# Performance work log

Hardware: AMD Instinct MI355X
Metric: run time of the kernel (lower is better)

## Reference

```python
import jax, jax.numpy as jnp
import numpy as np

NEG_INF = -1e6

def setup_inputs() -> dict:
    key = jax.random.key(0)
    ks = jax.random.split(key, 7)
    B, Q, K, D, H = 16, 64, 1024, 256, 128
    return {
        "queries": jax.random.normal(ks[0], (B, Q, D), dtype=jnp.float32),
        "keys": jax.random.normal(ks[1], (B, K, D), dtype=jnp.float32),
        "values": jax.random.normal(ks[2], (B, K, D), dtype=jnp.float32),
        "valid_lens": jax.random.randint(ks[3], (B,), 1, K + 1, dtype=jnp.int32),
        "W_q": jax.random.normal(ks[4], (D, H), dtype=jnp.float32) * (1.0 / np.sqrt(D)),
        "W_k": jax.random.normal(ks[5], (D, H), dtype=jnp.float32) * (1.0 / np.sqrt(D)),
        "w_v": jax.random.normal(ks[6], (H,), dtype=jnp.float32) * (1.0 / np.sqrt(H)),
    }

def reference(queries, keys, values, valid_lens, W_q, W_k, w_v):
    # project: [B,Q,H], [B,K,H]
    q = jnp.einsum('bqd,dh->bqh', queries, W_q)
    k = jnp.einsum('bkd,dh->bkh', keys, W_k)
    # broadcast add -> tanh -> score: [B,Q,K]
    features = jnp.tanh(q[:, :, None, :] + k[:, None, :, :])  # [B,Q,K,H]
    scores = jnp.einsum('bqkh,h->bqk', features, w_v)
    # masked softmax over key axis (valid_lens per batch)
    K_len = keys.shape[1]
    mask = jnp.arange(K_len)[None, None, :] < valid_lens[:, None, None]  # [B,1,K]
    scores = jnp.where(mask, scores, NEG_INF)
    attn = jax.nn.softmax(scores, axis=-1)
    # weighted sum of values: [B,Q,Dv]  (dropout p=0 -> identity)
    return jnp.einsum('bqk,bkd->bqd', attn, values)
```

## Files before the change

### kernel.cpp

```cpp
#include <hip/hip_runtime.h>

#define DDIM 256
#define HDIM 128
#define KLEN 1024
#define SCL 2.8853900817779268f

__global__ __launch_bounds__(256) void proj_kernel(
    const float* __restrict__ queries, const float* __restrict__ keys,
    const float* __restrict__ W_q, const float* __restrict__ W_k,
    float* __restrict__ Eq, float* __restrict__ Ek)
{
    __shared__ union {
        float a[64 * 64];
        float t[32][68];
    } sm;

    const int tid  = threadIdx.x;
    const int lane = tid & 63;
    const int wav  = tid >> 6;

    int blk = blockIdx.x;
    bool iskey; int b = 0, kc0 = 0, hb, row0;
    const float* in; const float* W;
    if (blk < 1024) {
        iskey = true;
        int xcd = blk & 7, s = blk >> 3;
        b = ((s >> 6) << 3) | xcd;
        int r6 = s & 63;
        kc0 = (r6 >> 2) << 6;
        hb  = (r6 & 3) << 5;
        row0 = b * KLEN + kc0;
        in = keys; W = W_k;
    } else {
        iskey = false;
        int qrb = blk - 1024;
        row0 = (qrb >> 2) << 6;
        hb   = (qrb & 3) << 5;
        in = queries; W = W_q;
    }

    const int hg8 = __builtin_amdgcn_readfirstlane(wav << 3);
    const float* Wu = W + hb + hg8;

    const int srow = tid >> 4;
    const int sgd  = tid & 15;
    const float* gsrc = in + (size_t)(row0 + srow) * DDIM + (sgd << 2);

    float4 pf0 = *(const float4*)(gsrc);
    float4 pf1 = *(const float4*)(gsrc + 16 * DDIM);
    float4 pf2 = *(const float4*)(gsrc + 32 * DDIM);
    float4 pf3 = *(const float4*)(gsrc + 48 * DDIM);

    float acc[8];
    #pragma unroll
    for (int c = 0; c < 8; c++) acc[c] = 0.f;

    const int w0 = (srow)      * 64 + ((sgd ^ ((srow)      & 7)) << 2);
    const int w1 = (srow + 16) * 64 + ((sgd ^ ((srow + 16) & 7)) << 2);
    const int w2 = (srow + 32) * 64 + ((sgd ^ ((srow + 32) & 7)) << 2);
    const int w3 = (srow + 48) * 64 + ((sgd ^ ((srow + 48) & 7)) << 2);

    for (int dt0 = 0; dt0 < DDIM; dt0 += 64) {
        *(float4*)(sm.a + w0) = pf0;
        *(float4*)(sm.a + w1) = pf1;
        *(float4*)(sm.a + w2) = pf2;
        *(float4*)(sm.a + w3) = pf3;
        __syncthreads();
        if (dt0 < DDIM - 64) {
            const float* g2 = gsrc + dt0 + 64;
            pf0 = *(const float4*)(g2);
            pf1 = *(const float4*)(g2 + 16 * DDIM);
            pf2 = *(const float4*)(g2 + 32 * DDIM);
            pf3 = *(const float4*)(g2 + 48 * DDIM);
        }
        const float* arow = sm.a + lane * 64;
        const int lx = lane & 7;
        #pragma unroll
        for (int d4 = 0; d4 < 64; d4 += 4) {
            float4 a = *(const float4*)(arow + ((((d4 >> 2)) ^ lx) << 2));
            const float* wr = Wu + (size_t)(dt0 + d4) * HDIM;
            #pragma unroll
            for (int c = 0; c < 8; c++) acc[c] = fmaf(a.x, wr[c],            acc[c]);
            #pragma unroll
            for (int c = 0; c < 8; c++) acc[c] = fmaf(a.y, wr[HDIM + c],     acc[c]);
            #pragma unroll
            for (int c = 0; c < 8; c++) acc[c] = fmaf(a.z, wr[2 * HDIM + c], acc[c]);
            #pragma unroll
            for (int c = 0; c < 8; c++) acc[c] = fmaf(a.w, wr[3 * HDIM + c], acc[c]);
        }
        __syncthreads();
    }

    float e[8];
    #pragma unroll
    for (int c = 0; c < 8; c++) e[c] = __builtin_amdgcn_exp2f(SCL * acc[c]);

    if (!iskey) {
        float* dst = Eq + (size_t)(row0 + lane) * HDIM + hb + hg8;
        *(float4*)(dst)     = make_float4(e[0], e[1], e[2], e[3]);
        *(float4*)(dst + 4) = make_float4(e[4], e[5], e[6], e[7]);
    } else {
        #pragma unroll
        for (int c = 0; c < 8; c++) sm.t[(wav << 3) + c][lane] = e[c];
        __syncthreads();
        float* dstb = Ek + (size_t)b * HDIM * KLEN + (size_t)hb * KLEN + kc0;
        #pragma unroll
        for (int i = 0; i < 2; i++) {
            int g = tid + (i << 8);
            int h = g >> 4, k4 = (g & 15) << 2;
            float4 o = *(const float4*)(&sm.t[h][k4]);
            *(float4*)(dstb + (size_t)h * KLEN + k4) = o;
        }
    }
}

__global__ __launch_bounds__(256) void score_av_kernel(
    const float* __restrict__ Eq, const float* __restrict__ Ek,
    const float* __restrict__ w_v, const int* __restrict__ valid_lens,
    const float* __restrict__ values,
    float* __restrict__ part, float* __restrict__ Tp)
{
    __shared__ union {
        struct {
            float4 eqw[4][HDIM];
            float  el[128][8];
        } p;
        float4 slab[4][8][64];
    } sm;
    __shared__ float tslab[4][8];

    const int tid = threadIdx.x;
    const int lane = tid & 63, wav = tid >> 6;
    int blk = blockIdx.x;
    int xcd = blk & 7, s = blk >> 3;
    int b = ((s >> 6) << 3) | xcd;
    int r = s & 63;
    int qt = r >> 3, kq = r & 7;
    int bq0 = b * 64 + qt * 8;
    int k0g = kq << 7;
    int vlen = valid_lens[b];

    #pragma unroll
    for (int i = 0; i < 2; i++) {
        int slot = tid + (i << 8);
        int w = slot >> 7, h = slot & 127;
        sm.p.eqw[w][h] = make_float4(
            Eq[(size_t)(bq0 + 2 * w) * HDIM + h],
            Eq[(size_t)(bq0 + 2 * w + 1) * HDIM + h],
            -2.0f * w_v[h], 0.f);
    }
    __syncthreads();

    const int kl = lane << 1;
    const float* ekp = Ek + (size_t)b * HDIM * KLEN + k0g + kl;
    float2 buf[8];
    #pragma unroll
    for (int j = 0; j < 8; j++)
        buf[j] = *(const float2*)(ekp + (size_t)j * KLEN);

    float2 acc0 = make_float2(0.f, 0.f), acc1 = make_float2(0.f, 0.f);
    for (int h0 = 0; h0 < HDIM; h0 += 8) {
        float2 nxt[8];
        if (h0 < HDIM - 8) {
            #pragma unroll
            for (int j = 0; j < 8; j++)
                nxt[j] = *(const float2*)(ekp + (size_t)(h0 + 8 + j) * KLEN);
        }
        #pragma unroll
        for (int j = 0; j < 8; j++) {
            float4 e = sm.p.eqw[wav][h0 + j];
            float2 ek = buf[j];
            acc0.x = fmaf(e.z, __builtin_amdgcn_rcpf(fmaf(e.x, ek.x, 1.f)), acc0.x);
            acc0.y = fmaf(e.z, __builtin_amdgcn_rcpf(fmaf(e.x, ek.y, 1.f)), acc0.y);
            acc1.x = fmaf(e.z, __builtin_amdgcn_rcpf(fmaf(e.y, ek.x, 1.f)), acc1.x);
            acc1.y = fmaf(e.z, __builtin_amdgcn_rcpf(fmaf(e.y, ek.y, 1.f)), acc1.y);
        }
        #pragma unroll
        for (int j = 0; j < 8; j++) buf[j] = nxt[j];
    }

    {
        int kg = k0g + kl;
        float e00 = (kg     < vlen) ? __expf(acc0.x) : 0.f;
        float e01 = (kg + 1 < vlen) ? __expf(acc0.y) : 0.f;
        float e10 = (kg     < vlen) ? __expf(acc1.x) : 0.f;
        float e11 = (kg + 1 < vlen) ? __expf(acc1.y) : 0.f;
        *(float2*)(&sm.p.el[kl][2 * wav])     = make_float2(e00, e10);
        *(float2*)(&sm.p.el[kl + 1][2 * wav]) = make_float2(e01, e11);
    }
    __syncthreads();

    int kw = wav << 5;
    int kg0 = k0g + kw;
    int cnt = vlen - kg0; cnt = cnt < 0 ? 0 : (cnt > 32 ? 32 : cnt);
    int cnt4 = (cnt + 3) & ~3;
    const float* vb = values + ((size_t)b * KLEN + kg0) * DDIM + (lane << 2);

    float4 acc[8];
    float acct[8];
    #pragma unroll
    for (int q = 0; q < 8; q++) { acc[q] = make_float4(0.f, 0.f, 0.f, 0.f); acct[q] = 0.f; }

    for (int k = 0; k < cnt4; k += 4) {
        #pragma unroll
        for (int j = 0; j < 4; j++) {
            float4 v  = *(const float4*)(vb + (size_t)(k + j) * DDIM);
            float4 p0 = *(const float4*)(&sm.p.el[kw + k + j][0]);
            float4 p1 = *(const float4*)(&sm.p.el[kw + k + j][4]);
            float pq[8] = {p0.x, p0.y, p0.z, p0.w, p1.x, p1.y, p1.z, p1.w};
            #pragma unroll
            for (int q = 0; q < 8; q++) {
                acc[q].x = fmaf(pq[q], v.x, acc[q].x);
                acc[q].y = fmaf(pq[q], v.y, acc[q].y);
                acc[q].z = fmaf(pq[q], v.z, acc[q].z);
                acc[q].w = fmaf(pq[q], v.w, acc[q].w);
                acct[q] += pq[q];
            }
        }
    }

    __syncthreads();
    #pragma unroll
    for (int q = 0; q < 8; q++) sm.slab[wav][q][lane] = acc[q];
    if (lane == 0) {
        #pragma unroll
        for (int q = 0; q < 8; q++) tslab[wav][q] = acct[q];
    }
    __syncthreads();
    #pragma unroll
    for (int e = 0; e < 2; e++) {
        int slot = (tid << 1) | e;
        int q = slot >> 6, d4 = slot & 63;
        float4 a = sm.slab[0][q][d4];
        #pragma unroll
        for (int g = 1; g < 4; g++) {
            float4 t = sm.slab[g][q][d4];
            a.x += t.x; a.y += t.y; a.z += t.z; a.w += t.w;
        }
        *(float4*)(part + ((size_t)kq * 1024 + bq0 + q) * DDIM + (d4 << 2)) = a;
    }
    if (tid < 8) {
        float t = tslab[0][tid] + tslab[1][tid] + tslab[2][tid] + tslab[3][tid];
        Tp[(size_t)kq * 1024 + bq0 + tid] = t;
    }
}

__global__ __launch_bounds__(256) void combine_kernel(
    const float* __restrict__ part, const float* __restrict__ Tp,
    float* __restrict__ out)
{
    int i = blockIdx.x * 256 + threadIdx.x;
    int row = i >> 6;
    const float4* p4 = (const float4*)part;
    float t = 0.f;
    #pragma unroll
    for (int j = 0; j < 8; j++) t += Tp[(size_t)j * 1024 + row];
    float inv = 1.0f / t;
    float4 a = p4[i];
    #pragma unroll
    for (int j = 1; j < 8; j++) {
        float4 v = p4[(size_t)j * 65536 + i];
        a.x += v.x; a.y += v.y; a.z += v.z; a.w += v.w;
    }
    a.x *= inv; a.y *= inv; a.z *= inv; a.w *= inv;
    ((float4*)out)[i] = a;
}

extern "C" void kernel_launch(void* const* d_in, const int* in_sizes, int n_in,
                              void* d_out, int out_size, void* d_ws, size_t ws_size,
                              hipStream_t stream) {
    const float* queries    = (const float*)d_in[0];
    const float* keys       = (const float*)d_in[1];
    const float* values     = (const float*)d_in[2];
    const int*   valid_lens = (const int*)d_in[3];
    const float* W_q        = (const float*)d_in[4];
    const float* W_k        = (const float*)d_in[5];
    const float* w_v        = (const float*)d_in[6];

    float* Eq   = (float*)d_ws;
    float* Ek   = Eq + 131072;
    float* part = Ek + 2097152;
    float* Tp   = part + 2097152;

    proj_kernel<<<1088, 256, 0, stream>>>(queries, keys, W_q, W_k, Eq, Ek);
    score_av_kernel<<<1024, 256, 0, stream>>>(Eq, Ek, w_v, valid_lens, values, part, Tp);
    combine_kernel<<<256, 256, 0, stream>>>(part, Tp, (float*)d_out);
}
```

Before: 136.2 us.

## Halve queries per score block, double grid, skip fully masked key chunks

The score/AV kernel now handles 4 queries per block instead of 8 and launches twice as many blocks, with a launch-bounds occupancy hint of 8 blocks. Blocks whose key chunk lies entirely past valid_len write zeros and exit early, skipping the tanh-score and value work. The cross-wave reduction becomes a serialized accumulate into shared memory with extra barriers, and each block now reloads its Ek and values tiles for half as many queries, which doubles that global traffic.

```diff
diff --git a/kernel.cpp b/kernel.cpp
--- a/kernel.cpp
+++ b/kernel.cpp
@@ -114,40 +114,44 @@
     }
 }
 
-__global__ __launch_bounds__(256) void score_av_kernel(
+__global__ __launch_bounds__(256, 8) void score_av_kernel(
     const float* __restrict__ Eq, const float* __restrict__ Ek,
     const float* __restrict__ w_v, const int* __restrict__ valid_lens,
     const float* __restrict__ values,
     float* __restrict__ part, float* __restrict__ Tp)
 {
     __shared__ union {
-        struct {
-            float4 eqw[4][HDIM];
-            float  el[128][8];
-        } p;
-        float4 slab[4][8][64];
-    } sm;
-    __shared__ float tslab[4][8];
+        float2 eqw[4][HDIM];
+        float  accbuf[4][256];
+    } u;
+    __shared__ float el[128][8];
+    __shared__ float tacc[4];
 
     const int tid = threadIdx.x;
     const int lane = tid & 63, wav = tid >> 6;
     int blk = blockIdx.x;
     int xcd = blk & 7, s = blk >> 3;
-    int b = ((s >> 6) << 3) | xcd;
-    int r = s & 63;
+    int b = ((s >> 7) << 3) | xcd;
+    int r = s & 127;
     int qt = r >> 3, kq = r & 7;
-    int bq0 = b * 64 + qt * 8;
+    int bq0 = b * 64 + qt * 4;
     int k0g = kq << 7;
     int vlen = valid_lens[b];
+
+    if (k0g >= vlen) {
+        int q = tid >> 6, d4 = tid & 63;
+        *(float4*)(part + ((size_t)kq * 1024 + bq0 + q) * DDIM + (d4 << 2)) =
+            make_float4(0.f, 0.f, 0.f, 0.f);
+        if (tid < 4) Tp[(size_t)kq * 1024 + bq0 + tid] = 0.f;
+        return;
+    }
 
     #pragma unroll
     for (int i = 0; i < 2; i++) {
         int slot = tid + (i << 8);
         int w = slot >> 7, h = slot & 127;
-        sm.p.eqw[w][h] = make_float4(
-            Eq[(size_t)(bq0 + 2 * w) * HDIM + h],
-            Eq[(size_t)(bq0 + 2 * w + 1) * HDIM + h],
-            -2.0f * w_v[h], 0.f);
+        u.eqw[w][h] = make_float2(Eq[(size_t)(bq0 + w) * HDIM + h],
+                                  -2.0f * w_v[h]);
     }
     __syncthreads();
 
@@ -158,7 +162,7 @@
     for (int j = 0; j < 8; j++)
         buf[j] = *(const float2*)(ekp + (size_t)j * KLEN);
 
-    float2 acc0 = make_float2(0.f, 0.f), acc1 = make_float2(0.f, 0.f);
+    float accx = 0.f, accy = 0.f;
     for (int h0 = 0; h0 < HDIM; h0 += 8) {
         float2 nxt[8];
         if (h0 < HDIM - 8) {
@@ -168,12 +172,10 @@
         }
         #pragma unroll
         for (int j = 0; j < 8; j++) {
-            float4 e = sm.p.eqw[wav][h0 + j];
+            float2 e  = u.eqw[wav][h0 + j];
             float2 ek = buf[j];
-            acc0.x = fmaf(e.z, __builtin_amdgcn_rcpf(fmaf(e.x, ek.x, 1.f)), acc0.x);
-            acc0.y = fmaf(e.z, __builtin_amdgcn_rcpf(fmaf(e.x, ek.y, 1.f)), acc0.y);
-            acc1.x = fmaf(e.z, __builtin_amdgcn_rcpf(fmaf(e.y, ek.x, 1.f)), acc1.x);
-            acc1.y = fmaf(e.z, __builtin_amdgcn_rcpf(fmaf(e.y, ek.y, 1.f)), acc1.y);
+            accx = fmaf(e.y, __builtin_amdgcn_rcpf(fmaf(e.x, ek.x, 1.f)), accx);
+            accy = fmaf(e.y, __builtin_amdgcn_rcpf(fmaf(e.x, ek.y, 1.f)), accy);
         }
         #pragma unroll
         for (int j = 0; j < 8; j++) buf[j] = nxt[j];
@@ -181,35 +183,29 @@
 
     {
         int kg = k0g + kl;
-        float e00 = (kg     < vlen) ? __expf(acc0.x) : 0.f;
-        float e01 = (kg + 1 < vlen) ? __expf(acc0.y) : 0.f;
-        float e10 = (kg     < vlen) ? __expf(acc1.x) : 0.f;
-        float e11 = (kg + 1 < vlen) ? __expf(acc1.y) : 0.f;
-        *(float2*)(&sm.p.el[kl][2 * wav])     = make_float2(e00, e10);
-        *(float2*)(&sm.p.el[kl + 1][2 * wav]) = make_float2(e01, e11);
+        el[kl][wav]     = (kg     < vlen) ? __expf(accx) : 0.f;
+        el[kl + 1][wav] = (kg + 1 < vlen) ? __expf(accy) : 0.f;
     }
     __syncthreads();
 
     int kw = wav << 5;
-    int kg0 = k0g + kw;
-    int cnt = vlen - kg0; cnt = cnt < 0 ? 0 : (cnt > 32 ? 32 : cnt);
+    int cnt = vlen - (k0g + kw); cnt = cnt < 0 ? 0 : (cnt > 32 ? 32 : cnt);
     int cnt4 = (cnt + 3) & ~3;
-    const float* vb = values + ((size_t)b * KLEN + kg0) * DDIM + (lane << 2);
-
-    float4 acc[8];
-    float acct[8];
-    #pragma unroll
-    for (int q = 0; q < 8; q++) { acc[q] = make_float4(0.f, 0.f, 0.f, 0.f); acct[q] = 0.f; }
+    const float* vb = values + ((size_t)b * KLEN + k0g + kw) * DDIM + (lane << 2);
+
+    float4 acc[4];
+    float acct[4];
+    #pragma unroll
+    for (int q = 0; q < 4; q++) { acc[q] = make_float4(0.f, 0.f, 0.f, 0.f); acct[q] = 0.f; }
 
     for (int k = 0; k < cnt4; k += 4) {
         #pragma unroll
         for (int j = 0; j < 4; j++) {
-            float4 v  = *(const float4*)(vb + (size_t)(k + j) * DDIM);
-            float4 p0 = *(const float4*)(&sm.p.el[kw + k + j][0]);
-            float4 p1 = *(const float4*)(&sm.p.el[kw + k + j][4]);
-            float pq[8] = {p0.x, p0.y, p0.z, p0.w, p1.x, p1.y, p1.z, p1.w};
-            #pragma unroll
-            for (int q = 0; q < 8; q++) {
+            float4 v = *(const float4*)(vb + (size_t)(k + j) * DDIM);
+            float4 p = *(const float4*)(&el[kw + k + j][0]);
+            float pq[4] = {p.x, p.y, p.z, p.w};
+            #pragma unroll
+            for (int q = 0; q < 4; q++) {
                 acc[q].x = fmaf(pq[q], v.x, acc[q].x);
                 acc[q].y = fmaf(pq[q], v.y, acc[q].y);
                 acc[q].z = fmaf(pq[q], v.z, acc[q].z);
@@ -220,29 +216,39 @@
     }
 
     __syncthreads();
-    #pragma unroll
-    for (int q = 0; q < 8; q++) sm.slab[wav][q][lane] = acc[q];
-    if (lane == 0) {
-        #pragma unroll
-        for (int q = 0; q < 8; q++) tslab[wav][q] = acct[q];
-    }
-    __syncthreads();
-    #pragma unroll
-    for (int e = 0; e < 2; e++) {
-        int slot = (tid << 1) | e;
-        int q = slot >> 6, d4 = slot & 63;
-        float4 a = sm.slab[0][q][d4];
-        #pragma unroll
-        for (int g = 1; g < 4; g++) {
-            float4 t = sm.slab[g][q][d4];
-            a.x += t.x; a.y += t.y; a.z += t.z; a.w += t.w;
-        }
-        *(float4*)(part + ((size_t)kq * 1024 + bq0 + q) * DDIM + (d4 << 2)) = a;
-    }
-    if (tid < 8) {
-        float t = tslab[0][tid] + tslab[1][tid] + tslab[2][tid] + tslab[3][tid];
-        Tp[(size_t)kq * 1024 + bq0 + tid] = t;
-    }
+    if (wav == 0) {
+        #pragma unroll
+        for (int q = 0; q < 4; q++)
+            *(float4*)(&u.accbuf[q][lane << 2]) = acc[q];
+        if (lane == 0) {
+            #pragma unroll
+            for (int q = 0; q < 4; q++) tacc[q] = acct[q];
+        }
+    }
+    __syncthreads();
+    #pragma unroll
+    for (int w = 1; w < 4; w++) {
+        if (wav == w) {
+            #pragma unroll
+            for (int q = 0; q < 4; q++) {
+                float4 t = *(const float4*)(&u.accbuf[q][lane << 2]);
+                t.x += acc[q].x; t.y += acc[q].y; t.z += acc[q].z; t.w += acc[q].w;
+                *(float4*)(&u.accbuf[q][lane << 2]) = t;
+            }
+            if (lane == 0) {
+                #pragma unroll
+                for (int q = 0; q < 4; q++) tacc[q] += acct[q];
+            }
+        }
+        __syncthreads();
+    }
+
+    {
+        int q = tid >> 6, d4 = tid & 63;
+        *(float4*)(part + ((size_t)kq * 1024 + bq0 + q) * DDIM + (d4 << 2)) =
+            *(const float4*)(&u.accbuf[q][d4 << 2]);
+    }
+    if (tid < 4) Tp[(size_t)kq * 1024 + bq0 + tid] = tacc[tid];
 }
 
 __global__ __launch_bounds__(256) void combine_kernel(
@@ -283,6 +289,6 @@
     float* Tp   = part + 2097152;
 
     proj_kernel<<<1088, 256, 0, stream>>>(queries, keys, W_q, W_k, Eq, Ek);
-    score_av_kernel<<<1024, 256, 0, stream>>>(Eq, Ek, w_v, valid_lens, values, part, Tp);
+    score_av_kernel<<<2048, 256, 0, stream>>>(Eq, Ek, w_v, valid_lens, values, part, Tp);
     combine_kernel<<<256, 256, 0, stream>>>(part, Tp, (float*)d_out);
 }
```

Measured after the change: 158.4 us. 1.16x slower.
